# Optimization experiments

Measured on AMD Instinct MI355X. Metric: run time of the kernel, lower is better.

Reference implementation:

```python
import jax, jax.numpy as jnp
import numpy as np

EPS = 1e-6
DIM = 384; HEADS = 6; POINTS = 4; LEVELS = 3; HIDDEN = 96
B = 2; H0 = 48; W0 = 48

def layernorm(x, w, b):
    m = jnp.mean(x, -1, keepdims=True)
    v = jnp.var(x, -1, keepdims=True)
    return (x - m) * jax.lax.rsqrt(v + EPS) * w + b

def make_ref_points(shapes):
    # normalized (x, y) pixel centers concatenated over levels -> [N, 2]
    pts = []
    for (Hl, Wl) in shapes:
        ry = (jnp.arange(Hl, dtype=jnp.float32) + 0.5) / Hl
        rx = (jnp.arange(Wl, dtype=jnp.float32) + 0.5) / Wl
        gy, gx = jnp.meshgrid(ry, rx, indexing='ij')
        pts.append(jnp.stack([gx.ravel(), gy.ravel()], -1))
    return jnp.concatenate(pts, 0)

def bilinear_gather(v, x, y, Hl, Wl):
    # v: [B, heads, Hl*Wl, c]; x, y: [B, heads, M] pixel coords
    # matches torch grid_sample(bilinear, align_corners=False, padding zeros)
    x0f = jnp.floor(x); y0f = jnp.floor(y)
    wx = (x - x0f)[..., None]; wy = (y - y0f)[..., None]
    x0 = x0f.astype(jnp.int32); y0 = y0f.astype(jnp.int32)
    def tap(yy, xx):
        valid = ((yy >= 0) & (yy < Hl) & (xx >= 0) & (xx < Wl)).astype(v.dtype)
        idx = jnp.clip(yy, 0, Hl - 1) * Wl + jnp.clip(xx, 0, Wl - 1)
        return jnp.take_along_axis(v, idx[..., None], axis=2) * valid[..., None]
    return (tap(y0, x0) * (1 - wx) * (1 - wy) + tap(y0, x0 + 1) * wx * (1 - wy)
            + tap(y0 + 1, x0) * (1 - wx) * wy + tap(y0 + 1, x0 + 1) * wx * wy)

def msdeform_attn(q, f, shapes, Wv, bv, Woff, boff, Watt, batt, Wout, bout):
    Bq, Nq, C = q.shape
    c = C // HEADS
    value = (f @ Wv + bv).reshape(Bq, -1, HEADS, c)
    off = (q @ Woff + boff).reshape(Bq, Nq, HEADS, LEVELS, POINTS, 2)
    att = jax.nn.softmax((q @ Watt + batt).reshape(Bq, Nq, HEADS, LEVELS * POINTS), -1)
    att = att.reshape(Bq, Nq, HEADS, LEVELS, POINTS)
    ref = make_ref_points(shapes)  # [Nq, 2]
    norm = jnp.array([[wl, hl] for (hl, wl) in shapes], dtype=q.dtype)  # [L, 2] = (W, H)
    loc = ref[None, :, None, None, None, :] + off / norm[None, None, None, :, None, :]
    starts = np.cumsum([0] + [h * w for (h, w) in shapes])
    out = jnp.zeros((Bq, Nq, HEADS, c), q.dtype)
    for l, (Hl, Wl) in enumerate(shapes):
        vl = value[:, starts[l]:starts[l + 1]].transpose(0, 2, 1, 3)  # [B,h,HW,c]
        ll = loc[:, :, :, l]  # [B,N,h,P,2]
        x = (ll[..., 0] * Wl - 0.5).transpose(0, 2, 1, 3).reshape(Bq, HEADS, Nq * POINTS)
        y = (ll[..., 1] * Hl - 0.5).transpose(0, 2, 1, 3).reshape(Bq, HEADS, Nq * POINTS)
        s = bilinear_gather(vl, x, y, Hl, Wl).reshape(Bq, HEADS, Nq, POINTS, c)
        out = out + jnp.einsum('bhnpc,bnhp->bnhc', s, att[:, :, :, l])
    return out.reshape(Bq, Nq, C) @ Wout + bout

def dwconv_levels(x, shapes, dw_w, dw_b):
    Bq, N, C = x.shape
    outs, s = [], 0
    for (Hl, Wl) in shapes:
        xi = x[:, s:s + Hl * Wl].reshape(Bq, Hl, Wl, C)
        yi = jax.lax.conv_general_dilated(xi, dw_w, (1, 1), 'SAME',
             dimension_numbers=('NHWC', 'HWIO', 'NHWC'), feature_group_count=C) + dw_b
        outs.append(yi.reshape(Bq, Hl * Wl, C))
        s += Hl * Wl
    return jnp.concatenate(outs, 1)

def setup_inputs():
    key = jax.random.key(0)
    ks = jax.random.split(key, 16)
    n = (H0 * W0) // 4
    N = 21 * n
    wfn = lambda k, s: 0.02 * jax.random.normal(k, s, jnp.float32)
    ones = lambda s: jnp.ones(s, jnp.float32)
    zeros = lambda s: jnp.zeros(s, jnp.float32)
    return {
        'query': jax.random.normal(ks[0], (B, N, DIM), jnp.float32),
        'reference_points': jax.random.uniform(ks[1], (B, N, 1, 2), dtype=jnp.float32),
        'feat': jax.random.normal(ks[2], (B, 4 * n, DIM), jnp.float32),
        'spatial_shapes': jnp.array([[2 * H0, 2 * W0], [H0, W0], [H0 // 2, W0 // 2]], jnp.int32),
        'level_start_index': jnp.array([0, 16 * n, 20 * n], jnp.int32),
        'H': H0, 'W': W0,
        'cti_qnorm_w': ones((DIM,)), 'cti_qnorm_b': zeros((DIM,)),
        'cti_fnorm_w': ones((DIM,)), 'cti_fnorm_b': zeros((DIM,)),
        'cf_qnorm_w': ones((DIM,)), 'cf_qnorm_b': zeros((DIM,)),
        'cf_fnorm_w': ones((DIM,)), 'cf_fnorm_b': zeros((DIM,)),
        'Wv': wfn(ks[3], (DIM, DIM)), 'bv': zeros((DIM,)),
        'Woff': wfn(ks[4], (DIM, HEADS * LEVELS * POINTS * 2)), 'boff': zeros((HEADS * LEVELS * POINTS * 2,)),
        'Watt': wfn(ks[5], (DIM, HEADS * LEVELS * POINTS)), 'batt': zeros((HEADS * LEVELS * POINTS,)),
        'Wout': wfn(ks[6], (DIM, DIM)), 'bout': zeros((DIM,)),
        'ffn_norm_w': ones((DIM,)), 'ffn_norm_b': zeros((DIM,)),
        'fc1_w': wfn(ks[7], (DIM, HIDDEN)), 'fc1_b': zeros((HIDDEN,)),
        'dw_w': wfn(ks[8], (3, 3, 1, HIDDEN)), 'dw_b': zeros((HIDDEN,)),
        'fc2_w': wfn(ks[9], (HIDDEN, DIM)), 'fc2_b': zeros((DIM,)),
    }

def reference(query, reference_points, feat, spatial_shapes, level_start_index, H, W,
              cti_qnorm_w, cti_qnorm_b, cti_fnorm_w, cti_fnorm_b,
              cf_qnorm_w, cf_qnorm_b, cf_fnorm_w, cf_fnorm_b,
              Wv, bv, Woff, boff, Watt, batt, Wout, bout,
              ffn_norm_w, ffn_norm_b, fc1_w, fc1_b, dw_w, dw_b, fc2_w, fc2_b):
    # NOTE: passed reference_points/spatial_shapes/level_start_index are ignored by
    # CTI_toC.forward; it recomputes them via deform_inputs_only_one(query, 16H, 16W).
    Bq, N, C = query.shape
    n = N // 21
    q = jnp.concatenate([query[:, :16 * n], query[:, 16 * n:20 * n] + feat, query[:, 20 * n:]], 1)
    shapes = [(2 * H, 2 * W), (H, W), (H // 2, W // 2)]
    qn = layernorm(q, cti_qnorm_w, cti_qnorm_b)
    fn = layernorm(q, cti_fnorm_w, cti_fnorm_b)
    aq = layernorm(qn, cf_qnorm_w, cf_qnorm_b)
    af = layernorm(fn, cf_fnorm_w, cf_fnorm_b)
    attn = msdeform_attn(aq, af, shapes, Wv, bv, Woff, boff, Watt, batt, Wout, bout)
    out = qn + attn
    h = layernorm(out, ffn_norm_w, ffn_norm_b) @ fc1_w + fc1_b
    h = dwconv_levels(h, shapes, dw_w, dw_b)
    h = jax.nn.gelu(h, approximate=False)
    h = h @ fc2_w + fc2_b
    return out + h
```

## Files before the change

kernel.cpp:

```cpp
#include <hip/hip_runtime.h>
#include <hip/hip_bf16.h>
#include <hip/hip_fp16.h>
#include <cstdint>
#include <cstddef>

#define NB 2
#define NTOK 12096
#define TOKS (NB * NTOK)
#define DIMC 384
#define NHEADS 6
#define CHD 64

typedef __attribute__((ext_vector_type(8))) __bf16 bf16x8;
typedef __attribute__((ext_vector_type(4))) float f32x4;

__device__ __forceinline__ float wave_reduce_add(float v) {
#pragma unroll
  for (int o = 32; o > 0; o >>= 1) v += __shfl_xor(v, o, 64);
  return v;
}

__device__ __forceinline__ float bf_lo(uint u) {
  union { uint i; float f; } c; c.i = u << 16; return c.f;
}
__device__ __forceinline__ float bf_hi(uint u) {
  union { uint i; float f; } c; c.i = u & 0xffff0000u; return c.f;
}
__device__ __forceinline__ ushort f2bf(float x) {
  union { __hip_bfloat16 b; ushort u; } c; c.b = __float2bfloat16(x); return c.u;
}

__device__ __forceinline__ void gload16(const ushort* g, ushort* l) {
  __builtin_amdgcn_global_load_lds(
      (const __attribute__((address_space(1))) uint*)g,
      (__attribute__((address_space(3))) uint*)l, 16, 0, 0);
}

__global__ __launch_bounds__(256) void convert_weights(
    const float* __restrict__ Wv, const float* __restrict__ Woff,
    const float* __restrict__ Watt, const float* __restrict__ Wo,
    const float* __restrict__ fc1, const float* __restrict__ fc2,
    const float* __restrict__ boff, const float* __restrict__ batt,
    const float* __restrict__ fc1b,
    __hip_bfloat16* __restrict__ Wvt, __hip_bfloat16* __restrict__ Wot,
    __hip_bfloat16* __restrict__ Wofat, __hip_bfloat16* __restrict__ fc1t,
    __hip_bfloat16* __restrict__ fc2t, float* __restrict__ bofat,
    float* __restrict__ fc1bp) {
  int id = blockIdx.x * 256 + threadIdx.x;
  if (id >= 384 * 384) return;
  int k = id % 384, n = id / 384;
  Wvt[(size_t)n * 384 + k] = __float2bfloat16(Wv[(size_t)k * 384 + n]);
  Wot[(size_t)n * 384 + k] = __float2bfloat16(Wo[(size_t)k * 384 + n]);
  if (n < 256) {
    float v = 0.f;
    if (n < 144) v = Woff[(size_t)k * 144 + n];
    else if (n < 216) v = Watt[(size_t)k * 72 + (n - 144)];
    Wofat[(size_t)n * 384 + k] = __float2bfloat16(v);
  }
  if (n < 128)
    fc1t[(size_t)n * 384 + k] = __float2bfloat16(n < 96 ? fc1[(size_t)k * 96 + n] : 0.f);
  if (k < 96)
    fc2t[(size_t)n * 96 + k] = __float2bfloat16(fc2[(size_t)k * 384 + n]);
  if (id < 256) bofat[id] = id < 144 ? boff[id] : (id < 216 ? batt[id - 144] : 0.f);
  if (id < 128) fc1bp[id] = id < 96 ? fc1b[id] : 0.f;
}

__global__ __launch_bounds__(256) void fused_ln3(
    const float* __restrict__ query, const float* __restrict__ feat,
    const float* __restrict__ w1, const float* __restrict__ b1,
    const float* __restrict__ w2, const float* __restrict__ b2,
    const float* __restrict__ w3, const float* __restrict__ b3,
    const float* __restrict__ w4, const float* __restrict__ b4,
    float* __restrict__ qn, __hip_bfloat16* __restrict__ aq,
    __hip_bfloat16* __restrict__ af) {
  int wid = (blockIdx.x * blockDim.x + threadIdx.x) >> 6;
  if (wid >= TOKS) return;
  int lane = threadIdx.x & 63;
  int bb = wid / NTOK;
  int nq = wid - bb * NTOK;

  float x[6];
  const float* qp = query + (size_t)wid * DIMC + lane;
#pragma unroll
  for (int i = 0; i < 6; ++i) x[i] = qp[64 * i];
  if (nq >= 9216 && nq < 11520) {
    const float* fp = feat + ((size_t)bb * 2304 + (nq - 9216)) * DIMC + lane;
#pragma unroll
    for (int i = 0; i < 6; ++i) x[i] += fp[64 * i];
  }

  float s = 0.f, ss = 0.f;
#pragma unroll
  for (int i = 0; i < 6; ++i) { s += x[i]; ss += x[i] * x[i]; }
  s = wave_reduce_add(s); ss = wave_reduce_add(ss);
  float mean = s * (1.f / DIMC);
  float rs = rsqrtf(ss * (1.f / DIMC) - mean * mean + 1e-6f);

  float qv[6], fv[6];
  float* qnp = qn + (size_t)wid * DIMC + lane;
#pragma unroll
  for (int i = 0; i < 6; ++i) {
    int e = lane + 64 * i;
    float xh = (x[i] - mean) * rs;
    qv[i] = xh * w1[e] + b1[e];
    fv[i] = xh * w2[e] + b2[e];
    qnp[64 * i] = qv[i];
  }

  s = 0.f; ss = 0.f;
#pragma unroll
  for (int i = 0; i < 6; ++i) { s += qv[i]; ss += qv[i] * qv[i]; }
  s = wave_reduce_add(s); ss = wave_reduce_add(ss);
  float m2 = s * (1.f / DIMC);
  float rs2 = rsqrtf(ss * (1.f / DIMC) - m2 * m2 + 1e-6f);
  __hip_bfloat16* aqp = aq + (size_t)wid * DIMC + lane;
#pragma unroll
  for (int i = 0; i < 6; ++i) {
    int e = lane + 64 * i;
    aqp[64 * i] = __float2bfloat16((qv[i] - m2) * rs2 * w3[e] + b3[e]);
  }

  s = 0.f; ss = 0.f;
#pragma unroll
  for (int i = 0; i < 6; ++i) { s += fv[i]; ss += fv[i] * fv[i]; }
  s = wave_reduce_add(s); ss = wave_reduce_add(ss);
  float m3 = s * (1.f / DIMC);
  float rs3 = rsqrtf(ss * (1.f / DIMC) - m3 * m3 + 1e-6f);
  __hip_bfloat16* afp = af + (size_t)wid * DIMC + lane;
#pragma unroll
  for (int i = 0; i < 6; ++i) {
    int e = lane + 64 * i;
    afp[64 * i] = __float2bfloat16((fv[i] - m3) * rs3 * w4[e] + b4[e]);
  }
}

__global__ __launch_bounds__(256) void ln_kernel(
    const float* __restrict__ x, const float* __restrict__ w,
    const float* __restrict__ b, __hip_bfloat16* __restrict__ y) {
  int wid = (blockIdx.x * blockDim.x + threadIdx.x) >> 6;
  if (wid >= TOKS) return;
  int lane = threadIdx.x & 63;
  float v[6];
  const float* xp = x + (size_t)wid * DIMC + lane;
#pragma unroll
  for (int i = 0; i < 6; ++i) v[i] = xp[64 * i];
  float s = 0.f, ss = 0.f;
#pragma unroll
  for (int i = 0; i < 6; ++i) { s += v[i]; ss += v[i] * v[i]; }
  s = wave_reduce_add(s); ss = wave_reduce_add(ss);
  float mean = s * (1.f / DIMC);
  float rs = rsqrtf(ss * (1.f / DIMC) - mean * mean + 1e-6f);
  __hip_bfloat16* yp = y + (size_t)wid * DIMC + lane;
#pragma unroll
  for (int i = 0; i < 6; ++i) {
    int e = lane + 64 * i;
    yp[64 * i] = __float2bfloat16((v[i] - mean) * rs * w[e] + b[e]);
  }
}

template <int EPI, int OUTBF16>
__global__ __launch_bounds__(256) void gemm_mfma(
    const __hip_bfloat16* __restrict__ A, const __hip_bfloat16* __restrict__ Wt,
    const float* __restrict__ bias, const float* __restrict__ R,
    void* __restrict__ Cv, int K, int Np) {
  __shared__ __align__(16) ushort As[128 * 32];
  __shared__ __align__(16) ushort Bs[128 * 32];
  const int tid = threadIdx.x;
  const int m0 = blockIdx.y * 128, n0 = blockIdx.x * 128;
  const int lane = tid & 63, wv = tid >> 6;
  const int wm = (wv >> 1) * 64, wn = (wv & 1) * 64;
  const int rl = lane & 15, kb = lane >> 4;

  const int c0 = wv * 64 + lane;
  const int c1 = c0 + 256;
  const int r0c = c0 >> 2, b0 = (c0 & 3) ^ (r0c & 3);
  const int r1c = c1 >> 2, b1 = (c1 & 3) ^ (r1c & 3);
  const ushort* gA0 = (const ushort*)A + (size_t)(m0 + r0c) * K + b0 * 8;
  const ushort* gA1 = (const ushort*)A + (size_t)(m0 + r1c) * K + b1 * 8;
  const ushort* gB0 = (const ushort*)Wt + (size_t)(n0 + r0c) * K + b0 * 8;
  const ushort* gB1 = (const ushort*)Wt + (size_t)(n0 + r1c) * K + b1 * 8;
  ushort* lA0 = &As[(size_t)wv * 512];
  ushort* lA1 = &As[(size_t)wv * 512 + 2048];
  ushort* lB0 = &Bs[(size_t)wv * 512];
  ushort* lB1 = &Bs[(size_t)wv * 512 + 2048];

  f32x4 acc[4][4] = {};

  for (int k0 = 0; k0 < K; k0 += 32) {
    gload16(gA0 + k0, lA0);
    gload16(gA1 + k0, lA1);
    gload16(gB0 + k0, lB0);
    gload16(gB1 + k0, lB1);
    __syncthreads();
    bf16x8 avf[4], bvf[4];
#pragma unroll
    for (int i = 0; i < 4; ++i) {
      int ra = wm + i * 16 + rl;
      avf[i] = *(const bf16x8*)&As[ra * 32 + ((kb ^ (ra & 3)) << 3)];
      int rb = wn + i * 16 + rl;
      bvf[i] = *(const bf16x8*)&Bs[rb * 32 + ((kb ^ (rb & 3)) << 3)];
    }
#pragma unroll
    for (int i = 0; i < 4; ++i)
#pragma unroll
      for (int j = 0; j < 4; ++j)
        acc[i][j] = __builtin_amdgcn_mfma_f32_16x16x32_bf16(avf[i], bvf[j],
                                                            acc[i][j], 0, 0, 0);
    __syncthreads();
  }

#pragma unroll
  for (int i = 0; i < 4; ++i) {
#pragma unroll
    for (int j = 0; j < 4; ++j) {
      int col = n0 + wn + j * 16 + rl;
      float bsv = bias[col];
#pragma unroll
      for (int r = 0; r < 4; ++r) {
        int row = m0 + wm + i * 16 + kb * 4 + r;
        size_t o = (size_t)row * Np + col;
        float v = acc[i][j][r] + bsv;
        if (EPI == 1) v += R[o];
        if (EPI == 2) v += ((const float*)Cv)[o];
        if (OUTBF16) ((__hip_bfloat16*)Cv)[o] = __float2bfloat16(v);
        else ((float*)Cv)[o] = v;
      }
    }
  }
}

__global__ __launch_bounds__(256) void msdeform_prep(
    const float* __restrict__ offatt, uint* __restrict__ taps) {
  int id = blockIdx.x * 256 + threadIdx.x;
  if (id >= TOKS * 72) return;
  int t = id / 72, r = id - t * 72;
  int h = r / 12, lp = r - h * 12;
  int l = lp >> 2;
  int nq = t % NTOK;

  int pos, Hq, Wq;
  if (nq < 9216)       { pos = nq;         Hq = 96; Wq = 96; }
  else if (nq < 11520) { pos = nq - 9216;  Hq = 48; Wq = 48; }
  else                 { pos = nq - 11520; Hq = 24; Wq = 24; }
  int iq = pos / Wq, jq = pos - iq * Wq;
  float refx = (jq + 0.5f) / (float)Wq;
  float refy = (iq + 0.5f) / (float)Hq;

  const float* lg = offatt + (size_t)t * 256 + 144 + h * 12;
  float mx = -1e30f;
#pragma unroll
  for (int i = 0; i < 12; ++i) mx = fmaxf(mx, lg[i]);
  float sden = 0.f;
#pragma unroll
  for (int i = 0; i < 12; ++i) sden += __expf(lg[i] - mx);
  float aw = __expf(lg[lp] - mx) / sden;

  float ox = offatt[(size_t)t * 256 + h * 24 + lp * 2 + 0];
  float oy = offatt[(size_t)t * 256 + h * 24 + lp * 2 + 1];

  int Wl = 96 >> l;

  float xx = refx * (float)Wl + ox - 0.5f;
  float yy = refy * (float)Wl + oy - 0.5f;
  float x0f = floorf(xx), y0f = floorf(yy);
  int x0 = (int)x0f, y0 = (int)y0f;
  float wx = xx - x0f, wy = yy - y0f;

  bool vx0 = (x0 >= 0) & (x0 < Wl), vx1 = (x0 + 1 >= 0) & (x0 + 1 < Wl);
  bool vy0 = (y0 >= 0) & (y0 < Wl), vy1 = (y0 + 1 >= 0) & (y0 + 1 < Wl);
  int x0c = min(max(x0, 0), Wl - 1), x1c = min(max(x0 + 1, 0), Wl - 1);
  int y0c = min(max(y0, 0), Wl - 1), y1c = min(max(y0 + 1, 0), Wl - 1);

  float w00 = (vy0 && vx0) ? aw * (1.f - wx) * (1.f - wy) : 0.f;
  float w01 = (vy0 && vx1) ? aw * wx * (1.f - wy) : 0.f;
  float w10 = (vy1 && vx0) ? aw * (1.f - wx) * wy : 0.f;
  float w11 = (vy1 && vx1) ? aw * wx * wy : 0.f;

  uint i00 = (uint)(y0c * Wl + x0c), i01 = (uint)(y0c * Wl + x1c);
  uint i10 = (uint)(y1c * Wl + x0c), i11 = (uint)(y1c * Wl + x1c);

  uint4 rec;
  rec.x = ((uint)f2bf(w00) << 16) | i00;
  rec.y = ((uint)f2bf(w01) << 16) | i01;
  rec.z = ((uint)f2bf(w10) << 16) | i10;
  rec.w = ((uint)f2bf(w11) << 16) | i11;
  *(uint4*)&taps[((size_t)(t * NHEADS + h)) * 48 + lp * 4] = rec;
}

__global__ __launch_bounds__(256) void msdeform_gather(
    const __hip_bfloat16* __restrict__ value, const uint* __restrict__ taps,
    __hip_bfloat16* __restrict__ samp) {
  const int NBLK = TOKS * NHEADS / 4;
  int bid = blockIdx.x;
  int swz = (bid & 7) * (NBLK / 8) + (bid >> 3);
  int wid = __builtin_amdgcn_readfirstlane(swz * 4 + ((int)threadIdx.x >> 6));
  int lane = threadIdx.x & 63;
  int g = lane >> 3, sub = lane & 7;
  int sub16 = sub * 16;

  int t = wid / NHEADS;
  int h = wid - t * NHEADS;
  int b = t / NTOK;

  const char* vb = (const char*)value + ((size_t)(b * NTOK) * DIMC + h * CHD) * 2;
  const char* vbl[3] = {vb, vb + 9216 * DIMC * 2, vb + 11520 * DIMC * 2};

  const uint* tp = taps + (size_t)wid * 48 + g;

  float acc[8] = {0.f, 0.f, 0.f, 0.f, 0.f, 0.f, 0.f, 0.f};
#pragma unroll
  for (int i = 0; i < 6; ++i) {
    uint rec = tp[i * 8];
    float wf = bf_hi(rec);
    uint off = (rec & 0x3fffu) * (uint)(DIMC * 2) + (uint)sub16;
    uint4 d = *(const uint4*)(vbl[i >> 1] + off);
    acc[0] = fmaf(wf, bf_lo(d.x), acc[0]);
    acc[1] = fmaf(wf, bf_hi(d.x), acc[1]);
    acc[2] = fmaf(wf, bf_lo(d.y), acc[2]);
    acc[3] = fmaf(wf, bf_hi(d.y), acc[3]);
    acc[4] = fmaf(wf, bf_lo(d.z), acc[4]);
    acc[5] = fmaf(wf, bf_hi(d.z), acc[5]);
    acc[6] = fmaf(wf, bf_lo(d.w), acc[6]);
    acc[7] = fmaf(wf, bf_hi(d.w), acc[7]);
  }

#pragma unroll
  for (int r = 0; r < 8; ++r) {
    acc[r] += __shfl_xor(acc[r], 8, 64);
    acc[r] += __shfl_xor(acc[r], 16, 64);
    acc[r] += __shfl_xor(acc[r], 32, 64);
  }

  if (lane < 8) {
    uint4 o;
    o.x = ((uint)f2bf(acc[1]) << 16) | f2bf(acc[0]);
    o.y = ((uint)f2bf(acc[3]) << 16) | f2bf(acc[2]);
    o.z = ((uint)f2bf(acc[5]) << 16) | f2bf(acc[4]);
    o.w = ((uint)f2bf(acc[7]) << 16) | f2bf(acc[6]);
    *(uint4*)((char*)samp + (size_t)wid * 128 + sub16) = o;
  }
}

__global__ __launch_bounds__(256) void dwconv_gelu(
    const __hip_bfloat16* __restrict__ x, const float* __restrict__ w,
    const float* __restrict__ bias, __hip_bfloat16* __restrict__ y) {
  int id = blockIdx.x * blockDim.x + threadIdx.x;
  if (id >= TOKS * 24) return;
  int g = id % 24;
  int tn = id / 24;
  int ch0 = g * 4;
  int b = tn / NTOK, nq = tn - b * NTOK;

  int pos, Hl, Wl, st;
  if (nq < 9216)       { pos = nq;         Hl = 96; Wl = 96; st = 0; }
  else if (nq < 11520) { pos = nq - 9216;  Hl = 48; Wl = 48; st = 9216; }
  else                 { pos = nq - 11520; Hl = 24; Wl = 24; st = 11520; }
  int i = pos / Wl, j = pos - i * Wl;

  f32x4 acc = *(const f32x4*)&bias[ch0];
#pragma unroll
  for (int di = 0; di < 3; ++di) {
#pragma unroll
    for (int dj = 0; dj < 3; ++dj) {
      int ii = i + di - 1, jj = j + dj - 1;
      if (ii >= 0 && ii < Hl && jj >= 0 && jj < Wl) {
        uint2 d = *(const uint2*)&x[((size_t)(b * NTOK + st + ii * Wl + jj)) * 128 + ch0];
        f32x4 wv = *(const f32x4*)&w[(di * 3 + dj) * 96 + ch0];
        acc[0] = fmaf(bf_lo(d.x), wv[0], acc[0]);
        acc[1] = fmaf(bf_hi(d.x), wv[1], acc[1]);
        acc[2] = fmaf(bf_lo(d.y), wv[2], acc[2]);
        acc[3] = fmaf(bf_hi(d.y), wv[3], acc[3]);
      }
    }
  }
  uint2 o;
  float g0 = 0.5f * acc[0] * (1.f + erff(acc[0] * 0.70710678f));
  float g1 = 0.5f * acc[1] * (1.f + erff(acc[1] * 0.70710678f));
  float g2 = 0.5f * acc[2] * (1.f + erff(acc[2] * 0.70710678f));
  float g3 = 0.5f * acc[3] * (1.f + erff(acc[3] * 0.70710678f));
  o.x = ((uint)f2bf(g1) << 16) | f2bf(g0);
  o.y = ((uint)f2bf(g3) << 16) | f2bf(g2);
  *(uint2*)((char*)y + (size_t)tn * 192 + ch0 * 2) = o;
}

extern "C" void kernel_launch(void* const* d_in, const int* in_sizes, int n_in,
                              void* d_out, int out_size, void* d_ws, size_t ws_size,
                              hipStream_t stream) {
  const float* query = (const float*)d_in[0];
  const float* feat   = (const float*)d_in[2];
  const float* cti_qw = (const float*)d_in[7];
  const float* cti_qb = (const float*)d_in[8];
  const float* cti_fw = (const float*)d_in[9];
  const float* cti_fb = (const float*)d_in[10];
  const float* cf_qw  = (const float*)d_in[11];
  const float* cf_qb  = (const float*)d_in[12];
  const float* cf_fw  = (const float*)d_in[13];
  const float* cf_fb  = (const float*)d_in[14];
  const float* Wv     = (const float*)d_in[15];
  const float* bv     = (const float*)d_in[16];
  const float* Woff   = (const float*)d_in[17];
  const float* boff   = (const float*)d_in[18];
  const float* Watt   = (const float*)d_in[19];
  const float* batt   = (const float*)d_in[20];
  const float* Wo     = (const float*)d_in[21];
  const float* bo     = (const float*)d_in[22];
  const float* ffw    = (const float*)d_in[23];
  const float* ffb    = (const float*)d_in[24];
  const float* fc1w   = (const float*)d_in[25];
  const float* fc1b   = (const float*)d_in[26];
  const float* dww    = (const float*)d_in[27];
  const float* dwb    = (const float*)d_in[28];
  const float* fc2w   = (const float*)d_in[29];
  const float* fc2b   = (const float*)d_in[30];
  float* out = (float*)d_out;

  char* ws = (char*)d_ws;
  float* qn = (float*)ws;
  __hip_bfloat16* aq  = (__hip_bfloat16*)(ws + 37158912);
  __hip_bfloat16* af  = (__hip_bfloat16*)(ws + 55738368);
  __hip_bfloat16* val = (__hip_bfloat16*)(ws + 74317824);
  float* offatt       = (float*)(ws + 92897280);
  char* wbase = ws + 117669888;
  __hip_bfloat16* Wvt   = (__hip_bfloat16*)(wbase + 0);
  __hip_bfloat16* Wot   = (__hip_bfloat16*)(wbase + 589824);
  __hip_bfloat16* Wofat = (__hip_bfloat16*)(wbase + 1179648);
  __hip_bfloat16* fc1t  = (__hip_bfloat16*)(wbase + 1376256);
  __hip_bfloat16* fc2t  = (__hip_bfloat16*)(wbase + 1474560);
  float* bofat          = (float*)(wbase + 1548288);
  float* fc1bp          = (float*)(wbase + 1549312);
  uint* taps = (uint*)(ws + 119220224);
  __hip_bfloat16* samp = af;
  __hip_bfloat16* lnf  = aq;
  __hip_bfloat16* h1   = (__hip_bfloat16*)offatt;
  __hip_bfloat16* h2   = (__hip_bfloat16*)(ws + 92897280 + 6193152);

  dim3 blk(256);

  convert_weights<<<576, blk, 0, stream>>>(Wv, Woff, Watt, Wo, fc1w, fc2w, boff,
                                           batt, fc1b, Wvt, Wot, Wofat, fc1t,
                                           fc2t, bofat, fc1bp);

  fused_ln3<<<TOKS / 4, blk, 0, stream>>>(query, feat, cti_qw, cti_qb, cti_fw,
                                          cti_fb, cf_qw, cf_qb, cf_fw, cf_fb,
                                          qn, aq, af);

  gemm_mfma<0, 1><<<dim3(3, 189), blk, 0, stream>>>(af, Wvt, bv, nullptr, val, 384, 384);
  gemm_mfma<0, 0><<<dim3(2, 189), blk, 0, stream>>>(aq, Wofat, bofat, nullptr, offatt, 384, 256);

  msdeform_prep<<<(TOKS * 72) / 256, blk, 0, stream>>>(offatt, taps);
  msdeform_gather<<<(TOKS * NHEADS) / 4, blk, 0, stream>>>(val, taps, samp);

  gemm_mfma<1, 0><<<dim3(3, 189), blk, 0, stream>>>(samp, Wot, bo, qn, out, 384, 384);

  ln_kernel<<<TOKS / 4, blk, 0, stream>>>(out, ffw, ffb, lnf);
  gemm_mfma<0, 1><<<dim3(1, 189), blk, 0, stream>>>(lnf, fc1t, fc1bp, nullptr, h1, 384, 128);
  dwconv_gelu<<<(TOKS * 24 + 255) / 256, blk, 0, stream>>>(h1, dww, dwb, h2);
  gemm_mfma<2, 0><<<dim3(3, 189), blk, 0, stream>>>(h2, fc2t, fc2b, nullptr, out, 96, 384);
}
```

Before: 204.7 us.

## Double-buffer GEMM LDS tiles, remap blocks per XCD, store qn as bf16

The GEMM now double-buffers its LDS tiles, issuing the next K-slice's global loads before computing on the current one, with one barrier per iteration instead of two. Work-group IDs are remapped so consecutive tiles land on the same XCD, which is meant to improve L2 reuse of shared A rows. The qn residual is now stored and read as bf16 rather than fp32, halving that traffic. The cost is lower residual precision and double the LDS use per block, which may reduce occupancy.

After: 190.5 us. 6.9% less time.

```diff
diff --git a/kernel.cpp b/kernel.cpp
--- a/kernel.cpp
+++ b/kernel.cpp
@@ -71,7 +71,7 @@
     const float* __restrict__ w2, const float* __restrict__ b2,
     const float* __restrict__ w3, const float* __restrict__ b3,
     const float* __restrict__ w4, const float* __restrict__ b4,
-    float* __restrict__ qn, __hip_bfloat16* __restrict__ aq,
+    __hip_bfloat16* __restrict__ qn, __hip_bfloat16* __restrict__ aq,
     __hip_bfloat16* __restrict__ af) {
   int wid = (blockIdx.x * blockDim.x + threadIdx.x) >> 6;
   if (wid >= TOKS) return;
@@ -97,14 +97,14 @@
   float rs = rsqrtf(ss * (1.f / DIMC) - mean * mean + 1e-6f);
 
   float qv[6], fv[6];
-  float* qnp = qn + (size_t)wid * DIMC + lane;
+  __hip_bfloat16* qnp = qn + (size_t)wid * DIMC + lane;
 #pragma unroll
   for (int i = 0; i < 6; ++i) {
     int e = lane + 64 * i;
     float xh = (x[i] - mean) * rs;
     qv[i] = xh * w1[e] + b1[e];
     fv[i] = xh * w2[e] + b2[e];
-    qnp[64 * i] = qv[i];
+    qnp[64 * i] = __float2bfloat16(qv[i]);
   }
 
   s = 0.f; ss = 0.f;
@@ -161,12 +161,20 @@
 template <int EPI, int OUTBF16>
 __global__ __launch_bounds__(256) void gemm_mfma(
     const __hip_bfloat16* __restrict__ A, const __hip_bfloat16* __restrict__ Wt,
-    const float* __restrict__ bias, const float* __restrict__ R,
-    void* __restrict__ Cv, int K, int Np) {
-  __shared__ __align__(16) ushort As[128 * 32];
-  __shared__ __align__(16) ushort Bs[128 * 32];
+    const float* __restrict__ bias, const void* __restrict__ Rv,
+    void* __restrict__ Cv, int K, int Np, int ntx) {
+  __shared__ __align__(16) ushort As[2 * 128 * 32];
+  __shared__ __align__(16) ushort Bs[2 * 128 * 32];
   const int tid = threadIdx.x;
-  const int m0 = blockIdx.y * 128, n0 = blockIdx.x * 128;
+
+  const int nwg = gridDim.x;
+  const int bid = blockIdx.x;
+  const int xcd = bid & 7, off = bid >> 3;
+  const int q = nwg >> 3, r = nwg & 7;
+  const int tile = (xcd < r ? xcd * (q + 1) : r * (q + 1) + (xcd - r) * q) + off;
+  const int tx = tile % ntx, ty = tile / ntx;
+  const int m0 = ty * 128, n0 = tx * 128;
+
   const int lane = tid & 63, wv = tid >> 6;
   const int wm = (wv >> 1) * 64, wn = (wv & 1) * 64;
   const int rl = lane & 15, kb = lane >> 4;
@@ -185,20 +193,31 @@
   ushort* lB1 = &Bs[(size_t)wv * 512 + 2048];
 
   f32x4 acc[4][4] = {};
-
-  for (int k0 = 0; k0 < K; k0 += 32) {
-    gload16(gA0 + k0, lA0);
-    gload16(gA1 + k0, lA1);
-    gload16(gB0 + k0, lB0);
-    gload16(gB1 + k0, lB1);
-    __syncthreads();
+  const int nt = K >> 5;
+
+  gload16(gA0, lA0);
+  gload16(gA1, lA1);
+  gload16(gB0, lB0);
+  gload16(gB1, lB1);
+  __syncthreads();
+
+  for (int t = 0; t < nt; ++t) {
+    const int cb = (t & 1) << 12;
+    const int nb = 4096 - cb;
+    if (t + 1 < nt) {
+      const int k1 = (t + 1) << 5;
+      gload16(gA0 + k1, lA0 + nb);
+      gload16(gA1 + k1, lA1 + nb);
+      gload16(gB0 + k1, lB0 + nb);
+      gload16(gB1 + k1, lB1 + nb);
+    }
     bf16x8 avf[4], bvf[4];
 #pragma unroll
     for (int i = 0; i < 4; ++i) {
       int ra = wm + i * 16 + rl;
-      avf[i] = *(const bf16x8*)&As[ra * 32 + ((kb ^ (ra & 3)) << 3)];
+      avf[i] = *(const bf16x8*)&As[cb + ra * 32 + ((kb ^ (ra & 3)) << 3)];
       int rb = wn + i * 16 + rl;
-      bvf[i] = *(const bf16x8*)&Bs[rb * 32 + ((kb ^ (rb & 3)) << 3)];
+      bvf[i] = *(const bf16x8*)&Bs[cb + rb * 32 + ((kb ^ (rb & 3)) << 3)];
     }
 #pragma unroll
     for (int i = 0; i < 4; ++i)
@@ -216,11 +235,11 @@
       int col = n0 + wn + j * 16 + rl;
       float bsv = bias[col];
 #pragma unroll
-      for (int r = 0; r < 4; ++r) {
-        int row = m0 + wm + i * 16 + kb * 4 + r;
+      for (int rr = 0; rr < 4; ++rr) {
+        int row = m0 + wm + i * 16 + kb * 4 + rr;
         size_t o = (size_t)row * Np + col;
-        float v = acc[i][j][r] + bsv;
-        if (EPI == 1) v += R[o];
+        float v = acc[i][j][rr] + bsv;
+        if (EPI == 1) v += __bfloat162float(((const __hip_bfloat16*)Rv)[o]);
         if (EPI == 2) v += ((const float*)Cv)[o];
         if (OUTBF16) ((__hip_bfloat16*)Cv)[o] = __float2bfloat16(v);
         else ((float*)Cv)[o] = v;
@@ -415,7 +434,7 @@
   float* out = (float*)d_out;
 
   char* ws = (char*)d_ws;
-  float* qn = (float*)ws;
+  __hip_bfloat16* qn  = (__hip_bfloat16*)ws;
   __hip_bfloat16* aq  = (__hip_bfloat16*)(ws + 37158912);
   __hip_bfloat16* af  = (__hip_bfloat16*)(ws + 55738368);
   __hip_bfloat16* val = (__hip_bfloat16*)(ws + 74317824);
@@ -444,16 +463,16 @@
                                           cti_fb, cf_qw, cf_qb, cf_fw, cf_fb,
                                           qn, aq, af);
 
-  gemm_mfma<0, 1><<<dim3(3, 189), blk, 0, stream>>>(af, Wvt, bv, nullptr, val, 384, 384);
-  gemm_mfma<0, 0><<<dim3(2, 189), blk, 0, stream>>>(aq, Wofat, bofat, nullptr, offatt, 384, 256);
+  gemm_mfma<0, 1><<<567, blk, 0, stream>>>(af, Wvt, bv, nullptr, val, 384, 384, 3);
+  gemm_mfma<0, 0><<<378, blk, 0, stream>>>(aq, Wofat, bofat, nullptr, offatt, 384, 256, 2);
 
   msdeform_prep<<<(TOKS * 72) / 256, blk, 0, stream>>>(offatt, taps);
   msdeform_gather<<<(TOKS * NHEADS) / 4, blk, 0, stream>>>(val, taps, samp);
 
-  gemm_mfma<1, 0><<<dim3(3, 189), blk, 0, stream>>>(samp, Wot, bo, qn, out, 384, 384);
+  gemm_mfma<1, 0><<<567, blk, 0, stream>>>(samp, Wot, bo, qn, out, 384, 384, 3);
 
   ln_kernel<<<TOKS / 4, blk, 0, stream>>>(out, ffw, ffb, lnf);
-  gemm_mfma<0, 1><<<dim3(1, 189), blk, 0, stream>>>(lnf, fc1t, fc1bp, nullptr, h1, 384, 128);
+  gemm_mfma<0, 1><<<189, blk, 0, stream>>>(lnf, fc1t, fc1bp, nullptr, h1, 384, 128, 1);
   dwconv_gelu<<<(TOKS * 24 + 255) / 256, blk, 0, stream>>>(h1, dww, dwb, h2);
-  gemm_mfma<2, 0><<<dim3(3, 189), blk, 0, stream>>>(h2, fc2t, fc2b, nullptr, out, 96, 384);
-}
+  gemm_mfma<2, 0><<<567, blk, 0, stream>>>(h2, fc2t, fc2b, nullptr, out, 96, 384, 3);
+}
```
